# Kernel tuning notes

Hardware: AMD Instinct MI355X
Metric: run time of the kernel (lower is better)

The kernel has to match this reference:

```python
import jax, jax.numpy as jnp
import numpy as np

NEW_INDEX = jnp.array([7, 0, 1, 6, 8, 2, 5, 4, 3], dtype=jnp.int32)
B, S, D, PF, LF, A = 65536, 20000, 300, 12, 8, 8
IN_DIM = PF + LF + 1  # 21
NCHW = ('NCHW', 'OIHW', 'NCHW')


def setup_inputs() -> dict:
    key = jax.random.key(0)
    ks = jax.random.split(key, 18)
    state = jax.random.randint(ks[0], (B,), 0, S)
    des = jax.random.randint(ks[1], (B,), 0, D)
    act = jax.random.randint(ks[2], (B,), 0, A)
    action_state_pad = jnp.concatenate(
        [jax.random.randint(ks[3], (S, A), 0, S), jnp.arange(S)[:, None]], axis=1)
    policy_mask_pad = jnp.concatenate(
        [jax.random.randint(ks[4], (S, A), 0, 2), jnp.zeros((S, 1), jnp.int32)], axis=1)
    path_feature = jax.random.normal(ks[5], (S, D, PF), jnp.float32)
    link_feature = jax.random.normal(ks[6], (S, LF), jnp.float32)
    w = lambda k, shp: jax.random.normal(k, shp, jnp.float32) * 0.05
    return {
        'state': state, 'des': des, 'act': act,
        'action_state_pad': action_state_pad, 'policy_mask_pad': policy_mask_pad,
        'path_feature': path_feature, 'link_feature': link_feature,
        'conv1_w': w(ks[7], (20, IN_DIM, 3, 3)), 'conv1_b': w(ks[8], (20,)),
        'conv2_w': w(ks[9], (30, 20, 2, 2)), 'conv2_b': w(ks[10], (30,)),
        'fc1_w': w(ks[11], (120, 30 + A)), 'fc1_b': w(ks[12], (120,)),
        'fc2_w': w(ks[13], (84, 120)), 'fc2_b': w(ks[14], (84,)),
        'fc3_w': w(ks[15], (1, 84)), 'fc3_b': w(ks[16], (1,)),
    }


def _process_features(state, des, action_state_pad, policy_mask_pad, path_feature, link_feature):
    neigh = action_state_pad[state]                       # [B, 9]
    npf = path_feature[neigh, des[:, None], :]            # [B, 9, PF]
    nef = link_feature[neigh]                             # [B, 9, LF]
    nmf = policy_mask_pad[state][..., None].astype(npf.dtype)  # [B, 9, 1]
    feat = jnp.concatenate([npf, nef, nmf], axis=-1)[:, NEW_INDEX, :]  # [B, 9, 21]
    x = feat.reshape(feat.shape[0], 3, 3, -1)             # [B, 3, 3, 21]
    return x.transpose(0, 3, 1, 2)                        # [B, 21, 3, 3]


def reference(state, des, act, action_state_pad, policy_mask_pad, path_feature,
              link_feature, conv1_w, conv1_b, conv2_w, conv2_b,
              fc1_w, fc1_b, fc2_w, fc2_b, fc3_w, fc3_b):
    lrelu = lambda v: jax.nn.leaky_relu(v, 0.2)
    x = _process_features(state, des, action_state_pad, policy_mask_pad,
                          path_feature, link_feature)
    x = jax.lax.conv_general_dilated(x, conv1_w, (1, 1), ((1, 1), (1, 1)),
                                     dimension_numbers=NCHW) + conv1_b[:, None, None]
    x = lrelu(x)                                          # [B, 20, 3, 3]
    x = jax.lax.reduce_window(x, -jnp.inf, jax.lax.max,
                              (1, 1, 2, 2), (1, 1, 1, 1), 'VALID')  # [B, 20, 2, 2]
    x = jax.lax.conv_general_dilated(x, conv2_w, (1, 1), 'VALID',
                                     dimension_numbers=NCHW) + conv2_b[:, None, None]
    x = lrelu(x).reshape(-1, 30)                          # [B, 30]
    x = jnp.concatenate([x, jax.nn.one_hot(act, A, dtype=x.dtype)], axis=1)  # [B, 38]
    x = lrelu(x @ fc1_w.T + fc1_b)
    x = lrelu(x @ fc2_w.T + fc2_b)
    return jax.nn.sigmoid(x @ fc3_w.T + fc3_b)            # [B, 1]
```

## Files before the change

kernel.cpp:

```cpp
#include <hip/hip_runtime.h>
#include <hip/hip_bf16.h>
#include <math.h>

#define DDIM   300
#define PFN    12
#define LFN    8
#define ICH    21
#define TPB    256
#define SPB    64
#define SLOT_DW 99
#define W1P    1980
#define W2N    2400
#define FW1H   2280
#define FW2H   5040
#define BIASN  339
#define OB1    0
#define OB2    20
#define OFB1   50
#define OFB2   170
#define OFW3   254
#define OFB3   338

__device__ __forceinline__ float lrelu(float v) { return v > 0.0f ? v : 0.2f * v; }

__device__ __forceinline__ unsigned int pack2(float a, float b) {
    union { __hip_bfloat162 h; unsigned int u; } cv;
    cv.h.x = __float2bfloat16(a);
    cv.h.y = __float2bfloat16(b);
    return cv.u;
}
__device__ __forceinline__ float bflo(unsigned int u) {
    union { unsigned int i; float f; } c; c.i = u << 16; return c.f;
}
__device__ __forceinline__ float bfhi(unsigned int u) {
    union { unsigned int i; float f; } c; c.i = u & 0xffff0000u; return c.f;
}

__device__ __forceinline__ float dot2bf(unsigned int a, unsigned int b, float c) {
    float d;
    asm("v_dot2_f32_bf16 %0, %1, %2, %3" : "=v"(d) : "v"(a), "v"(b), "v"(c));
    return d;
}

__device__ __forceinline__ void conv_acc2(float o[9], const unsigned int* __restrict__ w,
                                          const unsigned int fv[9]) {
#pragma unroll
    for (int t = 0; t < 9; ++t) {
        const int ky = t / 3 - 1, kx = t % 3 - 1;
        const unsigned int wv = w[t];
#pragma unroll
        for (int y = 0; y < 3; ++y) {
            const int iy = y + ky;
            if (iy < 0 || iy > 2) continue;
#pragma unroll
            for (int x = 0; x < 3; ++x) {
                const int ix = x + kx;
                if (ix < 0 || ix > 2) continue;
                o[y * 3 + x] = dot2bf(wv, fv[iy * 3 + ix], o[y * 3 + x]);
            }
        }
    }
}

__launch_bounds__(TPB, 2)
__global__ void disc_kernel(
    const int* __restrict__ state, const int* __restrict__ des,
    const int* __restrict__ act,
    const int* __restrict__ asp_g,
    const int* __restrict__ pmp_g,
    const float* __restrict__ path_feature,
    const float* __restrict__ link_feature,
    const float* __restrict__ w1, const float* __restrict__ b1,
    const float* __restrict__ w2, const float* __restrict__ b2,
    const float* __restrict__ fw1, const float* __restrict__ fb1,
    const float* __restrict__ fw2, const float* __restrict__ fb2,
    const float* __restrict__ fw3, const float* __restrict__ fb3,
    float* __restrict__ out, int n)
{
    __shared__ __align__(16) unsigned int w1p[W1P];
    __shared__ __align__(16) float w2s[W2N];
    __shared__ __align__(16) unsigned int fw1h[FW1H];
    __shared__ __align__(16) unsigned int fw2h[FW2H];
    __shared__ float bias[BIASN];
    __shared__ unsigned int feat[SPB * SLOT_DW];

    const int tid = threadIdx.x;

    {
        for (int i = tid; i < W1P; i += TPB) {
            const int oc = i / 99, r = i % 99, icp = r / 9, t = r % 9;
            const float lo = w1[(oc * ICH + 2 * icp) * 9 + t];
            const float hi = (icp < 10) ? w1[(oc * ICH + 2 * icp + 1) * 9 + t] : 0.0f;
            w1p[i] = pack2(lo, hi);
        }
        const float4* s2 = (const float4*)w2;  float4* d2 = (float4*)w2s;
        for (int i = tid; i < W2N / 4; i += TPB) d2[i] = s2[i];
        const float2* sf1 = (const float2*)fw1;
        for (int i = tid; i < FW1H; i += TPB) { const float2 v = sf1[i]; fw1h[i] = pack2(v.x, v.y); }
        const float2* sf2 = (const float2*)fw2;
        for (int i = tid; i < FW2H; i += TPB) { const float2 v = sf2[i]; fw2h[i] = pack2(v.x, v.y); }
        for (int i = tid; i < BIASN; i += TPB) {
            float v;
            if      (i < OB2)  v = b1[i];
            else if (i < OFB1) v = b2[i - OB2];
            else if (i < OFB2) v = fb1[i - OFB1];
            else if (i < OFW3) v = fb2[i - OFB2];
            else if (i < OFB3) v = fw3[i - OFW3];
            else               v = fb3[0];
            bias[i] = v;
        }
    }
    __syncthreads();

    const int lane4  = tid & 3;
    const int lsamp  = tid >> 2;
    const int sample = blockIdx.x * SPB + lsamp;
    if (sample >= n) return;

    const int s  = state[sample];
    const int d  = des[sample];
    const int ai = act[sample];

    const int* asp = asp_g + s * 9;
    const int* pmp = pmp_g + s * 9;
    unsigned int* fslot = feat + lsamp * SLOT_DW;

#pragma unroll
    for (int t = 0; t < 3; ++t) {
        const int p = lane4 + 4 * t;
        if (p < 9) {
            const int a  = (int)((0x345286107ULL >> (4 * p)) & 0xF);
            const int na = asp[a];
            const float m = (float)pmp[a];
            const float4* pf = (const float4*)(path_feature + (na * DDIM + d) * PFN);
            const float4 v0 = pf[0], v1 = pf[1], v2 = pf[2];
            const float4* lf = (const float4*)(link_feature + na * LFN);
            const float4 u0 = lf[0], u1 = lf[1];
            unsigned int* dst = fslot + p * 11;
            dst[0] = pack2(v0.x, v0.y); dst[1] = pack2(v0.z, v0.w);
            dst[2] = pack2(v1.x, v1.y); dst[3] = pack2(v1.z, v1.w);
            dst[4] = pack2(v2.x, v2.y); dst[5] = pack2(v2.z, v2.w);
            dst[6] = pack2(u0.x, u0.y); dst[7] = pack2(u0.z, u0.w);
            dst[8] = pack2(u1.x, u1.y); dst[9] = pack2(u1.z, u1.w);
            dst[10] = pack2(m, 0.0f);
        }
    }
    asm volatile("s_waitcnt lgkmcnt(0)" ::: "memory");

    const int oc0 = lane4 * 5;
    float o[5][9];
#pragma unroll
    for (int c = 0; c < 5; ++c) {
        const float bb = bias[OB1 + oc0 + c];
#pragma unroll
        for (int q = 0; q < 9; ++q) o[c][q] = bb;
    }

#pragma unroll 1
    for (int icp = 0; icp < 11; ++icp) {
        unsigned int fwd[9];
#pragma unroll
        for (int q = 0; q < 9; ++q) fwd[q] = fslot[q * 11 + icp];
        unsigned int wt[9];
#pragma unroll
        for (int c = 0; c < 5; ++c) {
            const unsigned int* wrow = w1p + (oc0 + c) * 99 + icp * 9;
#pragma unroll
            for (int t = 0; t < 9; ++t) wt[t] = wrow[t];
            conv_acc2(o[c], wt, fwd);
        }
    }

    float pooled[5][4];
#pragma unroll
    for (int c = 0; c < 5; ++c) {
        float v[9];
#pragma unroll
        for (int q = 0; q < 9; ++q) v[q] = lrelu(o[c][q]);
        pooled[c][0] = fmaxf(fmaxf(v[0], v[1]), fmaxf(v[3], v[4]));
        pooled[c][1] = fmaxf(fmaxf(v[1], v[2]), fmaxf(v[4], v[5]));
        pooled[c][2] = fmaxf(fmaxf(v[3], v[4]), fmaxf(v[6], v[7]));
        pooled[c][3] = fmaxf(fmaxf(v[4], v[5]), fmaxf(v[7], v[8]));
    }

    float x30[30];
#pragma unroll
    for (int j = 0; j < 30; ++j) {
        const float4* wr = (const float4*)(w2s + j * 80 + oc0 * 4);
        float acc = 0.0f;
#pragma unroll
        for (int c = 0; c < 5; ++c) {
            const float4 wv = wr[c];
            acc = fmaf(wv.x, pooled[c][0], acc);
            acc = fmaf(wv.y, pooled[c][1], acc);
            acc = fmaf(wv.z, pooled[c][2], acc);
            acc = fmaf(wv.w, pooled[c][3], acc);
        }
        acc += __shfl_xor(acc, 1, 64);
        acc += __shfl_xor(acc, 2, 64);
        x30[j] = lrelu(acc + bias[OB2 + j]);
    }

    unsigned int xp[15];
#pragma unroll
    for (int m = 0; m < 15; ++m) xp[m] = pack2(x30[2 * m], x30[2 * m + 1]);

    float h1[30];
    const int j0 = lane4 * 30;
    const int ohd   = (30 + ai) >> 1;
    const int ohodd = (30 + ai) & 1;
#pragma unroll
    for (int jj = 0; jj < 30; ++jj) {
        const unsigned int* wr = fw1h + (j0 + jj) * 19;
        const unsigned int uoh = wr[ohd];
        float acc = bias[OFB1 + j0 + jj] + (ohodd ? bfhi(uoh) : bflo(uoh));
#pragma unroll
        for (int m = 0; m < 15; ++m)
            acc = dot2bf(wr[m], xp[m], acc);
        h1[jj] = lrelu(acc);
    }

    unsigned int hp[15];
#pragma unroll
    for (int m = 0; m < 15; ++m) hp[m] = pack2(h1[2 * m], h1[2 * m + 1]);

    float z = bias[OFB3];
#pragma unroll 2
    for (int i = 0; i < 84; ++i) {
        const unsigned int* wp = fw2h + i * 60 + lane4 * 15;
        float a = 0.0f;
#pragma unroll
        for (int m = 0; m < 15; ++m)
            a = dot2bf(wp[m], hp[m], a);
        a += __shfl_xor(a, 1, 64);
        a += __shfl_xor(a, 2, 64);
        z = fmaf(bias[OFW3 + i], lrelu(a + bias[OFB2 + i]), z);
    }

    if (lane4 == 0)
        out[sample] = 1.0f / (1.0f + __expf(-z));
}

extern "C" void kernel_launch(void* const* d_in, const int* in_sizes, int n_in,
                              void* d_out, int out_size, void* d_ws, size_t ws_size,
                              hipStream_t stream) {
    const int*   state = (const int*)d_in[0];
    const int*   des   = (const int*)d_in[1];
    const int*   act   = (const int*)d_in[2];
    const int*   asp   = (const int*)d_in[3];
    const int*   pmp   = (const int*)d_in[4];
    const float* pathf = (const float*)d_in[5];
    const float* linkf = (const float*)d_in[6];
    const float* w1    = (const float*)d_in[7];
    const float* b1    = (const float*)d_in[8];
    const float* w2    = (const float*)d_in[9];
    const float* b2    = (const float*)d_in[10];
    const float* fw1   = (const float*)d_in[11];
    const float* fb1   = (const float*)d_in[12];
    const float* fw2   = (const float*)d_in[13];
    const float* fb2   = (const float*)d_in[14];
    const float* fw3   = (const float*)d_in[15];
    const float* fb3   = (const float*)d_in[16];

    const int n = in_sizes[0];
    dim3 grid((n + SPB - 1) / SPB), block(TPB);
    hipLaunchKernelGGL(disc_kernel, grid, block, 0, stream,
                       state, des, act, asp, pmp, pathf, linkf,
                       w1, b1, w2, b2, fw1, fb1, fw2, fb2, fw3, fb3,
                       (float*)d_out, n);
}
```

Before: 459.9 us.

## Pack conv2 weights to bf16 dot2 and raise block size to 384 threads

```diff
diff --git a/kernel.cpp b/kernel.cpp
--- a/kernel.cpp
+++ b/kernel.cpp
@@ -6,11 +6,11 @@
 #define PFN    12
 #define LFN    8
 #define ICH    21
-#define TPB    256
-#define SPB    64
+#define TPB    384
+#define SPB    96
 #define SLOT_DW 99
 #define W1P    1980
-#define W2N    2400
+#define W2P    1200
 #define FW1H   2280
 #define FW2H   5040
 #define BIASN  339
@@ -42,7 +42,7 @@
     return d;
 }
 
-__device__ __forceinline__ void conv_acc2(float o[9], const unsigned int* __restrict__ w,
+__device__ __forceinline__ void conv_acc2(float o[9], const unsigned int w[9],
                                           const unsigned int fv[9]) {
 #pragma unroll
     for (int t = 0; t < 9; ++t) {
@@ -62,7 +62,7 @@
     }
 }
 
-__launch_bounds__(TPB, 2)
+__launch_bounds__(TPB, 3)
 __global__ void disc_kernel(
     const int* __restrict__ state, const int* __restrict__ des,
     const int* __restrict__ act,
@@ -78,7 +78,7 @@
     float* __restrict__ out, int n)
 {
     __shared__ __align__(16) unsigned int w1p[W1P];
-    __shared__ __align__(16) float w2s[W2N];
+    __shared__ __align__(16) unsigned int w2p[W2P];
     __shared__ __align__(16) unsigned int fw1h[FW1H];
     __shared__ __align__(16) unsigned int fw2h[FW2H];
     __shared__ float bias[BIASN];
@@ -93,8 +93,10 @@
             const float hi = (icp < 10) ? w1[(oc * ICH + 2 * icp + 1) * 9 + t] : 0.0f;
             w1p[i] = pack2(lo, hi);
         }
-        const float4* s2 = (const float4*)w2;  float4* d2 = (float4*)w2s;
-        for (int i = tid; i < W2N / 4; i += TPB) d2[i] = s2[i];
+        for (int i = tid; i < W2P; i += TPB) {
+            const int j = i / 40, r = i % 40, oc = r / 2, h = r % 2;
+            w2p[i] = pack2(w2[j * 80 + oc * 4 + 2 * h], w2[j * 80 + oc * 4 + 2 * h + 1]);
+        }
         const float2* sf1 = (const float2*)fw1;
         for (int i = tid; i < FW1H; i += TPB) { const float2 v = sf1[i]; fw1h[i] = pack2(v.x, v.y); }
         const float2* sf2 = (const float2*)fw2;
@@ -171,30 +173,29 @@
         }
     }
 
-    float pooled[5][4];
+    unsigned int pp[5][2];
 #pragma unroll
     for (int c = 0; c < 5; ++c) {
         float v[9];
 #pragma unroll
         for (int q = 0; q < 9; ++q) v[q] = lrelu(o[c][q]);
-        pooled[c][0] = fmaxf(fmaxf(v[0], v[1]), fmaxf(v[3], v[4]));
-        pooled[c][1] = fmaxf(fmaxf(v[1], v[2]), fmaxf(v[4], v[5]));
-        pooled[c][2] = fmaxf(fmaxf(v[3], v[4]), fmaxf(v[6], v[7]));
-        pooled[c][3] = fmaxf(fmaxf(v[4], v[5]), fmaxf(v[7], v[8]));
+        const float p0 = fmaxf(fmaxf(v[0], v[1]), fmaxf(v[3], v[4]));
+        const float p1 = fmaxf(fmaxf(v[1], v[2]), fmaxf(v[4], v[5]));
+        const float p2 = fmaxf(fmaxf(v[3], v[4]), fmaxf(v[6], v[7]));
+        const float p3 = fmaxf(fmaxf(v[4], v[5]), fmaxf(v[7], v[8]));
+        pp[c][0] = pack2(p0, p1);
+        pp[c][1] = pack2(p2, p3);
     }
 
     float x30[30];
 #pragma unroll
     for (int j = 0; j < 30; ++j) {
-        const float4* wr = (const float4*)(w2s + j * 80 + oc0 * 4);
+        const unsigned int* wb = w2p + j * 40 + oc0 * 2;
         float acc = 0.0f;
 #pragma unroll
         for (int c = 0; c < 5; ++c) {
-            const float4 wv = wr[c];
-            acc = fmaf(wv.x, pooled[c][0], acc);
-            acc = fmaf(wv.y, pooled[c][1], acc);
-            acc = fmaf(wv.z, pooled[c][2], acc);
-            acc = fmaf(wv.w, pooled[c][3], acc);
+            acc = dot2bf(wb[2 * c],     pp[c][0], acc);
+            acc = dot2bf(wb[2 * c + 1], pp[c][1], acc);
         }
         acc += __shfl_xor(acc, 1, 64);
         acc += __shfl_xor(acc, 2, 64);
```

New measurement: 491.1 us. 6.8% more time.
